# Kernel tuning notes

Measured on AMD Instinct MI355X. Metric: run time of the kernel, lower is better.

## Reference

```python
import jax, jax.numpy as jnp
import numpy as np

B, N_VEC, D, C, N_W, N_CLASS, VOCAB = 16, 4096, 256, 256, 12, 10, 32
N_LINKS = N_W + 1


def _chord_cols(n_vec, n_links):
    # cols[i] = [i, (i+2^0)%n, (i+2^1)%n, ..., (i+2^(L-2))%n]
    i = np.arange(n_vec)[:, None]
    offs = np.concatenate([[0], 2 ** np.arange(n_links - 1)])[None, :]
    return ((i + offs) % n_vec).astype(np.int32)


def setup_inputs() -> dict:
    key = jax.random.key(0)
    ks = jax.random.split(key, 16)
    s = 0.02
    return {
        "tokens": jax.random.randint(ks[0], (B, N_VEC), 0, VOCAB),
        "cols": jnp.asarray(_chord_cols(N_VEC, N_LINKS)),
        "emb": jax.random.normal(ks[1], (VOCAB, D), jnp.float32) * s,
        "pos_emb": jax.random.normal(ks[2], (N_VEC, D), jnp.float32) * s,
        "g_w1": jax.random.normal(ks[3], (D, C), jnp.float32) * s,
        "g_b1": jnp.zeros((C,), jnp.float32),
        "g_w2": jax.random.normal(ks[4], (C, C), jnp.float32) * s,
        "g_b2": jnp.zeros((C,), jnp.float32),
        "fs_w1": jax.random.normal(ks[5], (N_W, D, D), jnp.float32) * s,
        "fs_b1": jnp.zeros((N_W, D), jnp.float32),
        "fs_w2": jax.random.normal(ks[6], (N_W, D, N_LINKS), jnp.float32) * s,
        "fs_b2": jnp.zeros((N_W, N_LINKS), jnp.float32),
        "fin_w": jax.random.normal(ks[7], (C, N_CLASS), jnp.float32) * s,
        "fin_b": jnp.zeros((N_CLASS,), jnp.float32),
    }


def reference(tokens, cols, emb, pos_emb, g_w1, g_b1, g_w2, g_b2,
              fs_w1, fs_b1, fs_w2, fs_b2, fin_w, fin_b):
    # token + positional embedding: [B, N, D]
    data = emb[tokens] + pos_emb[None, :, :]
    # g MLP -> V: [B, N, C]   (torch GELU = exact erf)
    V = jax.nn.gelu(data @ g_w1 + g_b1, approximate=False) @ g_w2 + g_b2
    res = V
    n_w = fs_w1.shape[0]
    for m in range(n_w):
        # per-edge weights: [B, N, L]
        W = jax.nn.gelu(data @ fs_w1[m] + fs_b1[m], approximate=False) @ fs_w2[m] + fs_b2[m]
        # chord spmm: V[b,i] = sum_l W[b,i,l] * V[b, cols[i,l]]
        Vg = V[:, cols, :]                       # [B, N, L, C]
        V = jnp.einsum('bnl,bnlc->bnc', W, Vg) + res
    cls = V[:, 0, :]                             # CLS pooling
    return cls @ fin_w + fin_b
```

## Files before the change

### kernel.cpp

```cpp
#include <hip/hip_runtime.h>
#include <hip/hip_bf16.h>
#include <math.h>

namespace {

constexpr int Bb   = 16;
constexpr int Nv   = 4096;
constexpr int NW   = 12;
constexpr int NL   = 13;
constexpr int NCLS = 10;
constexpr int BN   = Bb * Nv;

typedef __attribute__((ext_vector_type(8))) short short8;
typedef __attribute__((ext_vector_type(4))) float float4_t;

__device__ __forceinline__ float gelu_poly(float x) {
    float u = x * x;
    float p = fmaf(u, fmaf(u, fmaf(u, -2.374656431e-3f, 1.994711402e-2f),
                           -1.329807601e-1f), 7.978845608e-1f);
    return x * fmaf(x * p, 0.5f, 0.5f);
}
__device__ __forceinline__ float bflo(unsigned int u) {
    return __builtin_bit_cast(float, u << 16);
}
__device__ __forceinline__ float bfhi(unsigned int u) {
    return __builtin_bit_cast(float, u & 0xffff0000u);
}
__device__ __forceinline__ unsigned int f2bf(float f) {
    unsigned int x = __builtin_bit_cast(unsigned int, f);
    x += 0x7fff + ((x >> 16) & 1);
    return x >> 16;
}
__device__ __forceinline__ unsigned short f2bf16(float f) {
    return __builtin_bit_cast(unsigned short, __float2bfloat16(f));
}
__device__ __forceinline__ void gload16(const unsigned short* g, unsigned short* l) {
    __builtin_amdgcn_global_load_lds(
        (const __attribute__((address_space(1))) void*)g,
        (__attribute__((address_space(3))) void*)l, 16, 0, 0);
}
__device__ __forceinline__ int xcd_swz(int bid) {
    return (bid & 7) * 128 + (bid >> 3);
}


__global__ __launch_bounds__(256) void xbf_kernel(
    const int* __restrict__ tokens,
    const float* __restrict__ emb,
    const float* __restrict__ pos,
    unsigned int* __restrict__ Xbf)
{
    int i  = blockIdx.x * 256 + threadIdx.x;
    int p  = i & 127;
    int bn = i >> 7;
    int n  = bn & (Nv - 1);
    int t  = tokens[bn];
    const float2* e2 = (const float2*)(emb + (size_t)t * 256);
    const float2* p2 = (const float2*)(pos + (size_t)n * 256);
    float2 a = e2[p], b = p2[p];
    Xbf[i] = f2bf(a.x + b.x) | (f2bf(a.y + b.y) << 16);
}

__global__ __launch_bounds__(256) void wt_kernel(
    const float* __restrict__ g_w1,
    const float* __restrict__ g_w2,
    const float* __restrict__ fs_w1,
    const float* __restrict__ fs_w2,
    unsigned short* __restrict__ WT,
    unsigned short* __restrict__ W2T)
{
    int bid = blockIdx.x;
    int t = threadIdx.x;
    if (bid < 14 * 16) {
        int mat = bid >> 4;
        int k0  = (bid & 15) * 16;
        const float* src = (mat == 0) ? g_w1
                         : (mat == 1) ? g_w2
                         : fs_w1 + (size_t)(mat - 2) * 65536;
        unsigned short tmp[16];
#pragma unroll
        for (int j = 0; j < 16; ++j)
            tmp[j] = (unsigned short)f2bf(src[(size_t)(k0 + j) * 256 + t]);
        unsigned short* dst = WT + ((size_t)mat * 256 + t) * 256 + k0;
#pragma unroll
        for (int j = 0; j < 16; ++j) dst[j] = tmp[j];
    } else {
        int m = bid - 224;
        const float* src = fs_w2 + (size_t)m * 256 * NL;
        unsigned short* dst = W2T + (size_t)m * 4096;
#pragma unroll
        for (int i = 0; i < 16; ++i) {
            int idx = t + i * 256;
            int n = idx >> 8, k = idx & 255;
            dst[idx] = (n < NL) ? (unsigned short)f2bf(src[(size_t)k * NL + n]) : 0;
        }
    }
}

__device__ __forceinline__ void gemm1_core(
    const unsigned short* __restrict__ Xg,
    const unsigned short* __restrict__ Wg,
    int row0, int tid,
    unsigned short* Xs,
    unsigned short* Wls,
    float4_t acc[4][4])
{
    const int w = tid >> 6, lane = tid & 63;
    const int l15 = lane & 15, lg = lane >> 4;

    for (int k0 = 0; k0 < 256; k0 += 64) {
#pragma unroll
        for (int i = 0; i < 2; ++i) {
            int slotb = w * 128 + i * 64;
            int slot = slotb + lane;
            int row = slot >> 3, pu = slot & 7, lu = pu ^ (row & 7);
            gload16(Xg + (size_t)(row0 + row) * 256 + k0 + lu * 8, Xs + slotb * 8);
        }
#pragma unroll
        for (int i = 0; i < 8; ++i) {
            int slotb = w * 512 + i * 64;
            int slot = slotb + lane;
            int n = slot >> 3, pu = slot & 7, lu = pu ^ (n & 7);
            gload16(Wg + (size_t)n * 256 + k0 + lu * 8, Wls + slotb * 8);
        }
        __syncthreads();

#pragma unroll
        for (int ks = 0; ks < 2; ++ks) {
            short8 a[4], b[4];
#pragma unroll
            for (int fr = 0; fr < 4; ++fr) {
                int r = fr * 16 + l15;
                int off = r * 128 + (((lg + ks * 4) ^ (r & 7)) << 4);
                a[fr] = *(const short8*)((const char*)Xs + off);
            }
#pragma unroll
            for (int nt = 0; nt < 4; ++nt) {
                int n = w * 64 + nt * 16 + l15;
                int off = n * 128 + (((lg + ks * 4) ^ (n & 7)) << 4);
                b[nt] = *(const short8*)((const char*)Wls + off);
            }
#pragma unroll
            for (int fr = 0; fr < 4; ++fr)
#pragma unroll
                for (int nt = 0; nt < 4; ++nt)
                    acc[fr][nt] = __builtin_amdgcn_mfma_f32_16x16x32_bf16(
                        a[fr], b[nt], acc[fr][nt], 0, 0, 0);
        }
        __syncthreads();
    }
}

template<bool GELU>
__global__ __launch_bounds__(256) void gemm_act_kernel(
    const unsigned short* __restrict__ X,
    const unsigned short* __restrict__ WT,
    const float* __restrict__ bias,
    unsigned short* __restrict__ Y)
{
    __shared__ __align__(128) unsigned char smem[40960];
    unsigned short* Xs  = (unsigned short*)smem;
    unsigned short* Wls = (unsigned short*)(smem + 8192);

    const int row0 = xcd_swz(blockIdx.x) * 64;
    const int tid  = threadIdx.x;
    const int w = tid >> 6, lane = tid & 63;
    const int l15 = lane & 15, lg = lane >> 4;

    float4_t acc[4][4];
#pragma unroll
    for (int fr = 0; fr < 4; ++fr)
#pragma unroll
        for (int nt = 0; nt < 4; ++nt) acc[fr][nt] = (float4_t)0.f;

    gemm1_core(X, WT, row0, tid, Xs, Wls, acc);

#pragma unroll
    for (int nt = 0; nt < 4; ++nt) {
        int c = w * 64 + nt * 16 + l15;
        float bv = bias[c];
#pragma unroll
        for (int fr = 0; fr < 4; ++fr)
#pragma unroll
            for (int reg = 0; reg < 4; ++reg) {
                float v = acc[fr][nt][reg] + bv;
                if (GELU) v = gelu_poly(v);
                Y[(size_t)(row0 + fr * 16 + lg * 4 + reg) * 256 + c] = f2bf16(v);
            }
    }
}

__global__ __launch_bounds__(256) void fsmlp_kernel(
    const unsigned short* __restrict__ X,
    const unsigned short* __restrict__ WT,
    const unsigned short* __restrict__ W2T,
    const float* __restrict__ fs_b1,
    const float* __restrict__ fs_b2,
    float* __restrict__ Wall)
{
    __shared__ __align__(128) unsigned char smem[40960];
    unsigned short* Xs  = (unsigned short*)smem;
    unsigned short* Wls = (unsigned short*)(smem + 8192);
    unsigned short* Hs  = (unsigned short*)smem;
    unsigned short* W2s = (unsigned short*)(smem + 32768);

    const int bid  = (blockIdx.x & 7) * 1536 + (blockIdx.x >> 3);
    const int m    = bid % 12;
    const int row0 = (bid / 12) * 64;
    const int tid  = threadIdx.x;
    const int w = tid >> 6, lane = tid & 63;
    const int l15 = lane & 15, lg = lane >> 4;

    const unsigned short* Wg   = WT + (size_t)(2 + m) * 65536;
    const unsigned short* W2Tm = W2T + (size_t)m * 4096;
    const float* b1m = fs_b1 + (size_t)m * 256;
    const float* b2m = fs_b2 + (size_t)m * NL;
    float* Wallm = Wall + (size_t)m * BN * NL;

    float4_t acc[4][4];
#pragma unroll
    for (int fr = 0; fr < 4; ++fr)
#pragma unroll
        for (int nt = 0; nt < 4; ++nt) acc[fr][nt] = (float4_t)0.f;

    gemm1_core(X, Wg, row0, tid, Xs, Wls, acc);

    for (int u = tid; u < 13 * 32; u += 256) {
        int row = u >> 5, cu = u & 31;
        short8 v = *(const short8*)(W2Tm + row * 256 + cu * 8);
        *(short8*)(W2s + row * 256 + ((cu ^ (row & 7)) << 3)) = v;
    }

#pragma unroll
    for (int nt = 0; nt < 4; ++nt) {
        int c = w * 64 + nt * 16 + l15;
        float bv = b1m[c];
        int cu = c >> 3, cl = c & 7;
#pragma unroll
        for (int fr = 0; fr < 4; ++fr)
#pragma unroll
            for (int reg = 0; reg < 4; ++reg) {
                int row = fr * 16 + lg * 4 + reg;
                Hs[row * 256 + ((cu ^ (row & 7)) << 3) + cl] =
                    f2bf16(gelu_poly(acc[fr][nt][reg] + bv));
            }
    }
    __syncthreads();

    float4_t wacc = (float4_t)0.f;
#pragma unroll
    for (int kc = 0; kc < 8; ++kc) {
        int ua = (((kc * 4 + lg) ^ (l15 & 7)) << 3);
        short8 a = *(const short8*)(Hs + (w * 16 + l15) * 256 + ua);
        short8 b = *(const short8*)(W2s + l15 * 256 + ua);
        wacc = __builtin_amdgcn_mfma_f32_16x16x32_bf16(a, b, wacc, 0, 0, 0);
    }
    if (l15 < NL) {
        float b2v = b2m[l15];
#pragma unroll
        for (int reg = 0; reg < 4; ++reg)
            Wallm[(size_t)(row0 + w * 16 + lg * 4 + reg) * NL + l15]
                = wacc[reg] + b2v;
    }
}

__global__ __launch_bounds__(256) void chord_kernel(
    const unsigned short* __restrict__ Vprev,
    const uint2* __restrict__ res,
    const float* __restrict__ Wm,
    uint2* __restrict__ Vnext)
{
    __shared__ __align__(16) unsigned short Vs[96 * 256];
    __shared__ float Wmix[64][NL];

    const int bid  = xcd_swz(blockIdx.x);
    const int row0 = bid * 64;
    const int n0   = row0 & (Nv - 1);
    const int bb   = row0 & ~(Nv - 1);
    const int tid  = threadIdx.x;

    for (int e = tid; e < 64 * NL; e += 256)
        Wmix[0][e] = Wm[(size_t)row0 * NL + e];

#pragma unroll
    for (int i = 0; i < 12; ++i) {
        int slot = i * 256 + tid;
        int j = slot >> 5, cu = slot & 31;
        int gr = bb + ((n0 + j) & (Nv - 1));
        gload16(Vprev + (size_t)gr * 256 + cu * 8, Vs + slot * 8);
    }
    __syncthreads();

    const int p = tid & 63;
    const int w = tid >> 6;
    const uint2* V2 = (const uint2*)Vprev;

    for (int it = 0; it < 16; ++it) {
        const int r = w * 16 + it;
        const size_t rb = (size_t)(row0 + r) * 64;
        uint2 rv = res[rb + p];
        float a0 = bflo(rv.x), a1 = bfhi(rv.x);
        float a2 = bflo(rv.y), a3 = bfhi(rv.y);

        const unsigned short* lbase = Vs + r * 256 + p * 4;
#pragma unroll
        for (int l = 0; l < 7; ++l) {
            const int off = (l == 0) ? 0 : (1 << (l - 1));
            uint2 gv = *(const uint2*)(lbase + off * 256);
            float wv = Wmix[r][l];
            a0 += wv * bflo(gv.x);  a1 += wv * bfhi(gv.x);
            a2 += wv * bflo(gv.y);  a3 += wv * bfhi(gv.y);
        }
#pragma unroll
        for (int l = 7; l < NL; ++l) {
            const int off = 1 << (l - 1);
            int gr = bb + ((n0 + r + off) & (Nv - 1));
            uint2 gv = V2[(size_t)gr * 64 + p];
            float wv = Wmix[r][l];
            a0 += wv * bflo(gv.x);  a1 += wv * bfhi(gv.x);
            a2 += wv * bflo(gv.y);  a3 += wv * bfhi(gv.y);
        }
        uint2 o;
        o.x = f2bf(a0) | (f2bf(a1) << 16);
        o.y = f2bf(a2) | (f2bf(a3) << 16);
        Vnext[rb + p] = o;
    }
}

__global__ __launch_bounds__(256) void final_kernel(
    const unsigned short* __restrict__ Vfin,
    const float* __restrict__ fin_w,
    const float* __restrict__ fin_b,
    float* __restrict__ out)
{
    int t = threadIdx.x;
    if (t < Bb * NCLS) {
        int b = t / NCLS, o = t % NCLS;
        float a = fin_b[o];
        const unsigned short* v = Vfin + (size_t)b * Nv * 256;
        for (int k = 0; k < 256; ++k)
            a += __builtin_bit_cast(float, (unsigned int)v[k] << 16)
                 * fin_w[k * NCLS + o];
        out[t] = a;
    }
}

}

extern "C" void kernel_launch(void* const* d_in, const int* in_sizes, int n_in,
                              void* d_out, int out_size, void* d_ws, size_t ws_size,
                              hipStream_t stream) {
    const int*   tokens = (const int*)d_in[0];
    const float* emb    = (const float*)d_in[2];
    const float* pos    = (const float*)d_in[3];
    const float* g_w1   = (const float*)d_in[4];
    const float* g_b1   = (const float*)d_in[5];
    const float* g_w2   = (const float*)d_in[6];
    const float* g_b2   = (const float*)d_in[7];
    const float* fs_w1  = (const float*)d_in[8];
    const float* fs_b1  = (const float*)d_in[9];
    const float* fs_w2  = (const float*)d_in[10];
    const float* fs_b2  = (const float*)d_in[11];
    const float* fin_w  = (const float*)d_in[12];
    const float* fin_b  = (const float*)d_in[13];
    float* out = (float*)d_out;

    unsigned short* Xbf = (unsigned short*)d_ws;
    unsigned short* WT  = Xbf + (size_t)BN * 256;
    unsigned short* W2T = WT + (size_t)14 * 65536;
    unsigned short* res = W2T + (size_t)12 * 4096;
    unsigned short* Va  = res + (size_t)BN * 256;
    unsigned short* Vb  = Va + (size_t)BN * 256;
    float* Wall = (float*)(Vb + (size_t)BN * 256);

    xbf_kernel<<<BN * 128 / 256, 256, 0, stream>>>(tokens, emb, pos,
                                                   (unsigned int*)Xbf);
    wt_kernel<<<14 * 16 + 12, 256, 0, stream>>>(g_w1, g_w2, fs_w1, fs_w2,
                                                WT, W2T);

    gemm_act_kernel<true><<<1024, 256, 0, stream>>>(Xbf, WT, g_b1, Va);
    gemm_act_kernel<false><<<1024, 256, 0, stream>>>(Va, WT + 65536, g_b2, res);

    fsmlp_kernel<<<12288, 256, 0, stream>>>(Xbf, WT, W2T, fs_b1, fs_b2, Wall);

    const unsigned short* vp = res;
    for (int m = 0; m < NW; ++m) {
        unsigned short* vn = (m & 1) ? Vb : Va;
        chord_kernel<<<1024, 256, 0, stream>>>(
            vp, (const uint2*)res,
            Wall + (size_t)m * BN * NL, (uint2*)vn);
        vp = vn;
    }

    final_kernel<<<1, 256, 0, stream>>>(vp, fin_w, fin_b, out);
}
```

Measured before the change: 612.1 us.

## Enlarge GEMM row tiles to 128 with 8 waves and register-resident W2

The GEMM core now processes 128-row tiles with 512 threads arranged as a 2x4 wave grid, so each staged weight tile in LDS serves twice as many rows. This roughly halves global weight traffic per output row in the g-MLP and fs-MLP kernels, and launch grids shrink to match. In the fs-MLP kernel the small second-layer weights are loaded straight from global memory into registers instead of being staged through LDS. LDS per block grows (up to 64KB), which may limit resident blocks and raises register pressure.

After: 587.5 us. -4.0%, faster.

```diff
diff --git a/kernel.cpp b/kernel.cpp
--- a/kernel.cpp
+++ b/kernel.cpp
@@ -106,19 +106,20 @@
     float4_t acc[4][4])
 {
     const int w = tid >> 6, lane = tid & 63;
+    const int wr = w >> 2, wc = w & 3;
     const int l15 = lane & 15, lg = lane >> 4;
 
     for (int k0 = 0; k0 < 256; k0 += 64) {
 #pragma unroll
         for (int i = 0; i < 2; ++i) {
-            int slotb = w * 128 + i * 64;
+            int slotb = i * 512 + w * 64;
             int slot = slotb + lane;
             int row = slot >> 3, pu = slot & 7, lu = pu ^ (row & 7);
             gload16(Xg + (size_t)(row0 + row) * 256 + k0 + lu * 8, Xs + slotb * 8);
         }
 #pragma unroll
-        for (int i = 0; i < 8; ++i) {
-            int slotb = w * 512 + i * 64;
+        for (int i = 0; i < 4; ++i) {
+            int slotb = i * 512 + w * 64;
             int slot = slotb + lane;
             int n = slot >> 3, pu = slot & 7, lu = pu ^ (n & 7);
             gload16(Wg + (size_t)n * 256 + k0 + lu * 8, Wls + slotb * 8);
@@ -130,14 +131,14 @@
             short8 a[4], b[4];
 #pragma unroll
             for (int fr = 0; fr < 4; ++fr) {
-                int r = fr * 16 + l15;
-                int off = r * 128 + (((lg + ks * 4) ^ (r & 7)) << 4);
+                int r = wr * 64 + fr * 16 + l15;
+                int off = r * 128 + (((lg + ks * 4) ^ (l15 & 7)) << 4);
                 a[fr] = *(const short8*)((const char*)Xs + off);
             }
 #pragma unroll
             for (int nt = 0; nt < 4; ++nt) {
-                int n = w * 64 + nt * 16 + l15;
-                int off = n * 128 + (((lg + ks * 4) ^ (n & 7)) << 4);
+                int n = wc * 64 + nt * 16 + l15;
+                int off = n * 128 + (((lg + ks * 4) ^ (l15 & 7)) << 4);
                 b[nt] = *(const short8*)((const char*)Wls + off);
             }
 #pragma unroll
@@ -152,19 +153,20 @@
 }
 
 template<bool GELU>
-__global__ __launch_bounds__(256) void gemm_act_kernel(
+__global__ __launch_bounds__(512) void gemm_act_kernel(
     const unsigned short* __restrict__ X,
     const unsigned short* __restrict__ WT,
     const float* __restrict__ bias,
     unsigned short* __restrict__ Y)
 {
-    __shared__ __align__(128) unsigned char smem[40960];
+    __shared__ __align__(128) unsigned char smem[49152];
     unsigned short* Xs  = (unsigned short*)smem;
-    unsigned short* Wls = (unsigned short*)(smem + 8192);
-
-    const int row0 = xcd_swz(blockIdx.x) * 64;
+    unsigned short* Wls = (unsigned short*)(smem + 16384);
+
+    const int row0 = ((blockIdx.x & 7) * 64 + (blockIdx.x >> 3)) * 128;
     const int tid  = threadIdx.x;
     const int w = tid >> 6, lane = tid & 63;
+    const int wr = w >> 2, wc = w & 3;
     const int l15 = lane & 15, lg = lane >> 4;
 
     float4_t acc[4][4];
@@ -177,7 +179,7 @@
 
 #pragma unroll
     for (int nt = 0; nt < 4; ++nt) {
-        int c = w * 64 + nt * 16 + l15;
+        int c = wc * 64 + nt * 16 + l15;
         float bv = bias[c];
 #pragma unroll
         for (int fr = 0; fr < 4; ++fr)
@@ -185,12 +187,13 @@
             for (int reg = 0; reg < 4; ++reg) {
                 float v = acc[fr][nt][reg] + bv;
                 if (GELU) v = gelu_poly(v);
-                Y[(size_t)(row0 + fr * 16 + lg * 4 + reg) * 256 + c] = f2bf16(v);
+                Y[(size_t)(row0 + wr * 64 + fr * 16 + lg * 4 + reg) * 256 + c]
+                    = f2bf16(v);
             }
     }
 }
 
-__global__ __launch_bounds__(256) void fsmlp_kernel(
+__global__ __launch_bounds__(512) void fsmlp_kernel(
     const unsigned short* __restrict__ X,
     const unsigned short* __restrict__ WT,
     const unsigned short* __restrict__ W2T,
@@ -198,17 +201,17 @@
     const float* __restrict__ fs_b2,
     float* __restrict__ Wall)
 {
-    __shared__ __align__(128) unsigned char smem[40960];
+    __shared__ __align__(128) unsigned char smem[65536];
     unsigned short* Xs  = (unsigned short*)smem;
-    unsigned short* Wls = (unsigned short*)(smem + 8192);
+    unsigned short* Wls = (unsigned short*)(smem + 16384);
     unsigned short* Hs  = (unsigned short*)smem;
-    unsigned short* W2s = (unsigned short*)(smem + 32768);
-
-    const int bid  = (blockIdx.x & 7) * 1536 + (blockIdx.x >> 3);
+
+    const int bid  = (blockIdx.x & 7) * 768 + (blockIdx.x >> 3);
     const int m    = bid % 12;
-    const int row0 = (bid / 12) * 64;
+    const int row0 = (bid / 12) * 128;
     const int tid  = threadIdx.x;
     const int w = tid >> 6, lane = tid & 63;
+    const int wr = w >> 2, wc = w & 3;
     const int l15 = lane & 15, lg = lane >> 4;
 
     const unsigned short* Wg   = WT + (size_t)(2 + m) * 65536;
@@ -225,22 +228,21 @@
 
     gemm1_core(X, Wg, row0, tid, Xs, Wls, acc);
 
-    for (int u = tid; u < 13 * 32; u += 256) {
-        int row = u >> 5, cu = u & 31;
-        short8 v = *(const short8*)(W2Tm + row * 256 + cu * 8);
-        *(short8*)(W2s + row * 256 + ((cu ^ (row & 7)) << 3)) = v;
-    }
+    short8 b2[8];
+#pragma unroll
+    for (int kc = 0; kc < 8; ++kc)
+        b2[kc] = *(const short8*)(W2Tm + l15 * 256 + kc * 32 + lg * 8);
 
 #pragma unroll
     for (int nt = 0; nt < 4; ++nt) {
-        int c = w * 64 + nt * 16 + l15;
+        int c = wc * 64 + nt * 16 + l15;
         float bv = b1m[c];
         int cu = c >> 3, cl = c & 7;
 #pragma unroll
         for (int fr = 0; fr < 4; ++fr)
 #pragma unroll
             for (int reg = 0; reg < 4; ++reg) {
-                int row = fr * 16 + lg * 4 + reg;
+                int row = wr * 64 + fr * 16 + lg * 4 + reg;
                 Hs[row * 256 + ((cu ^ (row & 7)) << 3) + cl] =
                     f2bf16(gelu_poly(acc[fr][nt][reg] + bv));
             }
@@ -252,8 +254,7 @@
     for (int kc = 0; kc < 8; ++kc) {
         int ua = (((kc * 4 + lg) ^ (l15 & 7)) << 3);
         short8 a = *(const short8*)(Hs + (w * 16 + l15) * 256 + ua);
-        short8 b = *(const short8*)(W2s + l15 * 256 + ua);
-        wacc = __builtin_amdgcn_mfma_f32_16x16x32_bf16(a, b, wacc, 0, 0, 0);
+        wacc = __builtin_amdgcn_mfma_f32_16x16x32_bf16(a, b2[kc], wacc, 0, 0, 0);
     }
     if (l15 < NL) {
         float b2v = b2m[l15];
@@ -378,10 +379,10 @@
     wt_kernel<<<14 * 16 + 12, 256, 0, stream>>>(g_w1, g_w2, fs_w1, fs_w2,
                                                 WT, W2T);
 
-    gemm_act_kernel<true><<<1024, 256, 0, stream>>>(Xbf, WT, g_b1, Va);
-    gemm_act_kernel<false><<<1024, 256, 0, stream>>>(Va, WT + 65536, g_b2, res);
-
-    fsmlp_kernel<<<12288, 256, 0, stream>>>(Xbf, WT, W2T, fs_b1, fs_b2, Wall);
+    gemm_act_kernel<true><<<512, 512, 0, stream>>>(Xbf, WT, g_b1, Va);
+    gemm_act_kernel<false><<<512, 512, 0, stream>>>(Va, WT + 65536, g_b2, res);
+
+    fsmlp_kernel<<<6144, 512, 0, stream>>>(Xbf, WT, W2T, fs_b1, fs_b2, Wall);
 
     const unsigned short* vp = res;
     for (int m = 0; m < NW; ++m) {
```
